# Optimization experiments

Hardware: AMD Instinct MI355X
Metric: run time of the kernel (lower is better)

## Reference

```python
import jax, jax.numpy as jnp
import numpy as np

HEADS = 4
DIM_HEAD = 32
EPS = 1e-5


def setup_inputs() -> dict:
    key = jax.random.key(0)
    ks = jax.random.split(key, 3)
    b, c, h, w = 32, 128, 128, 128
    hidden = HEADS * DIM_HEAD  # 128
    x = jax.random.normal(ks[0], (b, c, h, w), dtype=jnp.float32)
    Wqkv = jax.random.normal(ks[1], (3 * hidden, c), dtype=jnp.float32) * (1.0 / np.sqrt(c))
    Wout = jax.random.normal(ks[2], (c, hidden), dtype=jnp.float32) * (1.0 / np.sqrt(hidden))
    bout = jnp.zeros((c,), dtype=jnp.float32)
    g = jnp.ones((c,), dtype=jnp.float32)
    return {"x": x, "Wqkv": Wqkv, "Wout": Wout, "bout": bout, "g": g}


def reference(x, Wqkv, Wout, bout, g):
    b, c, h, w = x.shape
    n = h * w
    scale = DIM_HEAD ** -0.5
    # 1x1 conv (no bias) == channel GEMM
    qkv = jnp.einsum('oc,bchw->bohw', Wqkv, x)  # [b, 3*hidden, h, w]
    q, k, v = jnp.split(qkv, 3, axis=1)
    # b (h d) x y -> b h d n
    def to_heads(t):
        return t.reshape(b, HEADS, DIM_HEAD, n)
    q, k, v = to_heads(q), to_heads(k), to_heads(v)
    q = jax.nn.softmax(q, axis=-2) * scale   # softmax over per-head channel dim
    k = jax.nn.softmax(k, axis=-1)           # softmax over token dim
    v = v / n
    ctx = jnp.einsum('bhdn,bhen->bhde', k, v)   # [b, heads, d, e]
    out = jnp.einsum('bhde,bhdn->bhen', ctx, q)  # [b, heads, e, n]
    out = out.reshape(b, HEADS * DIM_HEAD, h, w)
    # output 1x1 conv with bias
    y = jnp.einsum('oc,bchw->bohw', Wout, out) + bout[None, :, None, None]
    # LayerNorm over channel dim (biased variance)
    mean = jnp.mean(y, axis=1, keepdims=True)
    var = jnp.var(y, axis=1, keepdims=True)
    return (y - mean) * jax.lax.rsqrt(var + EPS) * g[None, :, None, None]
```

## Files before the change

kernel.cpp:

```cpp
#include <hip/hip_runtime.h>
#include <math.h>


#define NCHUNK 64

typedef __attribute__((ext_vector_type(8))) short short8;
typedef __attribute__((ext_vector_type(4))) float f32x4;

__device__ __forceinline__ uint bf16r(float f) {
    uint u = __float_as_uint(f);
    return (u + 0x7FFFu + ((u >> 16) & 1u)) >> 16;
}
__device__ __forceinline__ float bf16f(uint h) { return __uint_as_float(h << 16); }
__device__ __forceinline__ uint2 bsplit(float f) {
    uint h = bf16r(f);
    float r = f - bf16f(h);
    return make_uint2(h, bf16r(r));
}
__device__ __forceinline__ uint2 bsplit_t(float f) {
    uint u = __float_as_uint(f);
    uint uh = u & 0xFFFF0000u;
    float r = f - __uint_as_float(uh);
    return make_uint2(uh >> 16, __float_as_uint(r) >> 16);
}
__device__ __forceinline__ uint bpack_t(float f) {
    uint u = __float_as_uint(f);
    uint uh = u & 0xFFFF0000u;
    float r = f - __uint_as_float(uh);
    return (uh >> 16) | (__float_as_uint(r) & 0xFFFF0000u);
}
__device__ __forceinline__ uint bpack(float f) {
    uint2 s = bsplit(f);
    return s.x | (s.y << 16);
}
__device__ __forceinline__ short8 lo8(uint4 a, uint4 b) {
    uint4 r;
    r.x = (a.x & 0xFFFFu) | (a.y << 16);
    r.y = (a.z & 0xFFFFu) | (a.w << 16);
    r.z = (b.x & 0xFFFFu) | (b.y << 16);
    r.w = (b.z & 0xFFFFu) | (b.w << 16);
    return __builtin_bit_cast(short8, r);
}
__device__ __forceinline__ short8 hi8(uint4 a, uint4 b) {
    uint4 r;
    r.x = (a.x >> 16) | (a.y & 0xFFFF0000u);
    r.y = (a.z >> 16) | (a.w & 0xFFFF0000u);
    r.z = (b.x >> 16) | (b.y & 0xFFFF0000u);
    r.w = (b.z >> 16) | (b.w & 0xFFFF0000u);
    return __builtin_bit_cast(short8, r);
}

__global__ __launch_bounds__(256)
void wsplit(const float* __restrict__ W, ushort* __restrict__ Wh,
            ushort* __restrict__ Wl, int n)
{
    const int base = (blockIdx.x * 256 + threadIdx.x) * 4;
    if (base + 3 < n) {
        const float4 f = *(const float4*)(W + base);
        const uint2 a = bsplit(f.x), b2 = bsplit(f.y), c = bsplit(f.z), d = bsplit(f.w);
        ushort4 hh; hh.x = (ushort)a.x; hh.y = (ushort)b2.x; hh.z = (ushort)c.x; hh.w = (ushort)d.x;
        ushort4 ll; ll.x = (ushort)a.y; ll.y = (ushort)b2.y; ll.z = (ushort)c.y; ll.w = (ushort)d.y;
        *(ushort4*)(Wh + base) = hh;
        *(ushort4*)(Wl + base) = ll;
    }
}

#define MFMA(A, B, C) __builtin_amdgcn_mfma_f32_16x16x32_bf16((A), (B), (C), 0, 0, 0)

__global__ __launch_bounds__(512, 1)
void la_k1(const float* __restrict__ x,
           const ushort* __restrict__ Wh, const ushort* __restrict__ Wl,
           float* __restrict__ Spart, float* __restrict__ Zpart)
{
    __shared__ __align__(16) char smb[163840];

    const int tid = threadIdx.x;
    const int b = blockIdx.y, chunk = blockIdx.x;
    const int w = tid >> 6, l = tid & 63;
    const int l15 = l & 15, lg = l >> 4;

    {
#pragma unroll
        for (int it = 0; it < 16; ++it) {
            const int q = tid + 512 * it;
            const int region = q >> 12;
            const int lin = (q & 4095) * 16;
            const int r = lin >> 8;
            const int dst = (region << 16) + (lin ^ ((r & 7) << 4));
            const ushort* src = (region ? Wl : Wh) + 128 * 128 + (lin >> 1);
            *(uint4*)(&smb[dst]) = *(const uint4*)src;
        }
    }

    f32x4 s2[2];
#pragma unroll
    for (int i = 0; i < 2; ++i) s2[i] = (f32x4){0.f, 0.f, 0.f, 0.f};
    float zrow[4];
#pragma unroll
    for (int i = 0; i < 4; ++i) zrow[i] = 0.f;

    const int hh = w >> 1, eh = w & 1;

    for (int t = 0; t < 8; ++t) {
        const int p0 = chunk * 256 + t * 32;
        {
            const float* xb = x + (size_t)b * 128 * 16384 + p0;
            const int cp = tid >> 3, j = tid & 7;
            const int pb = j * 4, c = cp * 2;
            const float4 a = *(const float4*)(xb + (size_t)c * 16384 + pb);
            const float4 bq = *(const float4*)(xb + (size_t)(c + 1) * 16384 + pb);
            const float av[4] = {a.x, a.y, a.z, a.w};
            const float bv[4] = {bq.x, bq.y, bq.z, bq.w};
#pragma unroll
            for (int pp = 0; pp < 4; ++pp) {
                const uint2 s0 = bsplit_t(av[pp]);
                const uint2 s1 = bsplit_t(bv[pp]);
                const int p = pb + pp;
                const int byt = (p * 256 + c * 2) ^ (((p ^ (p >> 3)) & 7) << 4);
                *(uint*)(&smb[131072 + byt])        = s0.x | (s1.x << 16);
                *(uint*)(&smb[131072 + 8192 + byt]) = s0.y | (s1.y << 16);
            }
        }
        __syncthreads();

        f32x4 acc[2][2];
#pragma unroll
        for (int rt = 0; rt < 2; ++rt)
#pragma unroll
            for (int ct = 0; ct < 2; ++ct) acc[rt][ct] = (f32x4){0.f, 0.f, 0.f, 0.f};
#pragma unroll
        for (int ks = 0; ks < 4; ++ks) {
            short8 Bh[2], Bl[2];
#pragma unroll
            for (int ct = 0; ct < 2; ++ct) {
                const int p = ct * 16 + l15;
                const int byt = (p * 256 + (ks * 32 + lg * 8) * 2) ^ (((p ^ (p >> 3)) & 7) << 4);
                Bh[ct] = *(const short8*)(&smb[131072 + byt]);
                Bl[ct] = *(const short8*)(&smb[131072 + 8192 + byt]);
            }
#pragma unroll
            for (int rt = 0; rt < 2; ++rt) {
                const int r = (w + rt * 8) * 16 + l15;
                const int abyt = (r * 256 + (ks * 32 + lg * 8) * 2) ^ ((r & 7) << 4);
                const short8 Ah_ = *(const short8*)(&smb[abyt]);
                const short8 Al_ = *(const short8*)(&smb[65536 + abyt]);
#pragma unroll
                for (int ct = 0; ct < 2; ++ct) {
                    acc[rt][ct] = MFMA(Ah_, Bh[ct], acc[rt][ct]);
                    acc[rt][ct] = MFMA(Ah_, Bl[ct], acc[rt][ct]);
                    acc[rt][ct] = MFMA(Al_, Bh[ct], acc[rt][ct]);
                }
            }
        }
        __syncthreads();

#pragma unroll
        for (int rt = 0; rt < 2; ++rt) {
            const bool isk = (rt == 0);
#pragma unroll
            for (int ct = 0; ct < 2; ++ct) {
                const int p = ct * 16 + l15;
#pragma unroll
                for (int i = 0; i < 4; ++i) {
                    float val = acc[rt][ct][i];
                    if (isk) {
                        val = expf(val);
                        zrow[i] += val;
                    }
                    const int r = w * 16 + lg * 4 + i;
                    const int byt = (r * 128 + p * 4) ^ ((r & 7) << 4);
                    *(uint*)(&smb[131072 + (isk ? 0 : 16384) + byt]) = bpack_t(val);
                }
            }
        }
        __syncthreads();

        {
            short8 A2h[2], A2l[2], B2h, B2l;
#pragma unroll
            for (int rt2 = 0; rt2 < 2; ++rt2) {
                const int r = hh * 32 + rt2 * 16 + l15;
                const int b0 = (r * 128 + lg * 32) ^ ((r & 7) << 4);
                const int b1 = (r * 128 + lg * 32 + 16) ^ ((r & 7) << 4);
                const uint4 q0 = *(const uint4*)(&smb[131072 + b0]);
                const uint4 q1 = *(const uint4*)(&smb[131072 + b1]);
                A2h[rt2] = lo8(q0, q1);
                A2l[rt2] = hi8(q0, q1);
            }
            {
                const int rv = hh * 32 + eh * 16 + l15;
                const int c0 = (rv * 128 + lg * 32) ^ ((rv & 7) << 4);
                const int c1 = (rv * 128 + lg * 32 + 16) ^ ((rv & 7) << 4);
                const uint4 r0 = *(const uint4*)(&smb[131072 + 16384 + c0]);
                const uint4 r1 = *(const uint4*)(&smb[131072 + 16384 + c1]);
                B2h = lo8(r0, r1);
                B2l = hi8(r0, r1);
            }
#pragma unroll
            for (int rt2 = 0; rt2 < 2; ++rt2) {
                s2[rt2] = MFMA(A2h[rt2], B2h, s2[rt2]);
                s2[rt2] = MFMA(A2h[rt2], B2l, s2[rt2]);
                s2[rt2] = MFMA(A2l[rt2], B2h, s2[rt2]);
            }
        }
        __syncthreads();
    }

    const size_t sbase = (((size_t)b * NCHUNK + chunk) * 4 + hh) * 1024;
#pragma unroll
    for (int rt2 = 0; rt2 < 2; ++rt2)
#pragma unroll
        for (int i = 0; i < 4; ++i) {
            const int d = rt2 * 16 + lg * 4 + i;
            const int e = eh * 16 + l15;
            Spart[sbase + d * 32 + e] = s2[rt2][i];
        }

#pragma unroll
    for (int i = 0; i < 4; ++i) {
        float z = zrow[i];
        z += __shfl_xor(z, 1, 64);
        z += __shfl_xor(z, 2, 64);
        z += __shfl_xor(z, 4, 64);
        z += __shfl_xor(z, 8, 64);
        if (l15 == 0)
            Zpart[((size_t)b * NCHUNK + chunk) * 128 + w * 16 + lg * 4 + i] = z;
    }
}

__global__ __launch_bounds__(256, 1)
void la_k1_reduce(const float* __restrict__ Spart, const float* __restrict__ Zpart,
                  uint* __restrict__ ctxT)
{
    const int tid = threadIdx.x;
    const int b  = blockIdx.x >> 2;
    const int hh = blockIdx.x & 3;
    const int d  = tid >> 3;
    const int e0 = (tid & 7) << 2;
    float sx = 0.f, sy = 0.f, sz = 0.f, sw = 0.f, z = 0.f;
    for (int ch = 0; ch < NCHUNK; ++ch) {
        const size_t base = (((size_t)b * NCHUNK + ch) * 4 + hh) * 32 + d;
        const float4 v = *(const float4*)(Spart + base * 32 + e0);
        sx += v.x; sy += v.y; sz += v.z; sw += v.w;
        z += Zpart[base];
    }
    const float inv = 1.0f / (z * 16384.0f);
    const size_t tb = (((size_t)b * 4 + hh) * 32) * 32 + d;
    ctxT[tb + (size_t)(e0 + 0) * 32] = bpack(sx * inv);
    ctxT[tb + (size_t)(e0 + 1) * 32] = bpack(sy * inv);
    ctxT[tb + (size_t)(e0 + 2) * 32] = bpack(sz * inv);
    ctxT[tb + (size_t)(e0 + 3) * 32] = bpack(sw * inv);
}

__device__ __forceinline__ int xswz64(int p, int cbyte) {
    return (p * 256 + cbyte) ^ (((p ^ (p >> 3)) & 7) << 4);
}

__global__ __launch_bounds__(256, 2)
void la_k2(const float* __restrict__ x,
           const ushort* __restrict__ Wqh, const ushort* __restrict__ Wql,
           const ushort* __restrict__ Woh, const ushort* __restrict__ Wol,
           const float* __restrict__ bout, const float* __restrict__ g,
           const uint* __restrict__ ctxT, float* __restrict__ outg)
{
    __shared__ __align__(16) char smb[66560];

    const int tid = threadIdx.x;
    const int b = blockIdx.y, chunk = blockIdx.x;
    const int p0 = chunk * 64;
    const int w = tid >> 6, l = tid & 63;
    const int l15 = l & 15, lg = l >> 4;
    const int ch2 = w >> 1;
    const int rp  = w & 1;

    short8 AqH[2][4], AqL[2][4];
#pragma unroll
    for (int t_ = 0; t_ < 2; ++t_)
#pragma unroll
        for (int ks = 0; ks < 4; ++ks) {
            const size_t aoff = (size_t)((2 * w + t_) * 16 + l15) * 128 + ks * 32 + lg * 8;
            AqH[t_][ks] = *(const short8*)(Wqh + aoff);
            AqL[t_][ks] = *(const short8*)(Wql + aoff);
        }

    {
        const float* xb = x + (size_t)b * 128 * 16384 + p0;
        const int j = tid & 15, gq = tid >> 4;
        const int pb = j * 4;
#pragma unroll
        for (int u = 0; u < 2; ++u) {
            const int cb = gq * 4 + u * 64;
            const float4 xv0 = *(const float4*)(xb + (size_t)(cb + 0) * 16384 + pb);
            const float4 xv1 = *(const float4*)(xb + (size_t)(cb + 1) * 16384 + pb);
            const float4 xv2 = *(const float4*)(xb + (size_t)(cb + 2) * 16384 + pb);
            const float4 xv3 = *(const float4*)(xb + (size_t)(cb + 3) * 16384 + pb);
            float rc[4][4];
            rc[0][0] = xv0.x; rc[0][1] = xv0.y; rc[0][2] = xv0.z; rc[0][3] = xv0.w;
            rc[1][0] = xv1.x; rc[1][1] = xv1.y; rc[1][2] = xv1.z; rc[1][3] = xv1.w;
            rc[2][0] = xv2.x; rc[2][1] = xv2.y; rc[2][2] = xv2.z; rc[2][3] = xv2.w;
            rc[3][0] = xv3.x; rc[3][1] = xv3.y; rc[3][2] = xv3.z; rc[3][3] = xv3.w;
#pragma unroll
            for (int pp = 0; pp < 4; ++pp) {
                const uint2 s0 = bsplit_t(rc[0][pp]);
                const uint2 s1 = bsplit_t(rc[1][pp]);
                const uint2 s2u = bsplit_t(rc[2][pp]);
                const uint2 s3 = bsplit_t(rc[3][pp]);
                const int p = pb + pp;
                const int byt = xswz64(p, cb * 2);
                *(uint2*)(&smb[byt])         = make_uint2(s0.x | (s1.x << 16), s2u.x | (s3.x << 16));
                *(uint2*)(&smb[16384 + byt]) = make_uint2(s0.y | (s1.y << 16), s2u.y | (s3.y << 16));
            }
        }
    }
    __syncthreads();

    f32x4 qacc[2][4];
#pragma unroll
    for (int t_ = 0; t_ < 2; ++t_)
#pragma unroll
        for (int ct = 0; ct < 4; ++ct) qacc[t_][ct] = (f32x4){0.f, 0.f, 0.f, 0.f};
#pragma unroll
    for (int ks = 0; ks < 4; ++ks) {
#pragma unroll
        for (int ct = 0; ct < 4; ++ct) {
            const int p = ct * 16 + l15;
            const int byt = xswz64(p, (ks * 32 + lg * 8) * 2);
            const short8 Bh_ = *(const short8*)(&smb[byt]);
            const short8 Bl_ = *(const short8*)(&smb[16384 + byt]);
#pragma unroll
            for (int t_ = 0; t_ < 2; ++t_) {
                qacc[t_][ct] = MFMA(AqH[t_][ks], Bh_, qacc[t_][ct]);
                qacc[t_][ct] = MFMA(AqH[t_][ks], Bl_, qacc[t_][ct]);
                qacc[t_][ct] = MFMA(AqL[t_][ks], Bh_, qacc[t_][ct]);
            }
        }
    }

    {
#pragma unroll
        for (int ct = 0; ct < 4; ++ct) {
            const int p = ct * 16 + l15;
            float vv[2][4];
            float m = -1e30f;
#pragma unroll
            for (int t_ = 0; t_ < 2; ++t_)
#pragma unroll
                for (int i = 0; i < 4; ++i) {
                    vv[t_][i] = qacc[t_][ct][i];
                    m = fmaxf(m, vv[t_][i]);
                }
            m = fmaxf(m, __shfl_xor(m, 16, 64));
            m = fmaxf(m, __shfl_xor(m, 32, 64));
            float s = 0.f;
#pragma unroll
            for (int t_ = 0; t_ < 2; ++t_)
#pragma unroll
                for (int i = 0; i < 4; ++i) {
                    vv[t_][i] = expf(vv[t_][i] - m);
                    s += vv[t_][i];
                }
            s += __shfl_xor(s, 16, 64);
            s += __shfl_xor(s, 32, 64);
            const float inv = 0.17677669529663687f / s;
            const int basep = (w * 64 + p) * 128;
            const int swzq = (p & 7) << 4;
#pragma unroll
            for (int t_ = 0; t_ < 2; ++t_) {
                uint4 pk;
                pk.x = bpack_t(vv[t_][0] * inv);
                pk.y = bpack_t(vv[t_][1] * inv);
                pk.z = bpack_t(vv[t_][2] * inv);
                pk.w = bpack_t(vv[t_][3] * inv);
                *(uint4*)(&smb[32768 + ((basep + (t_ * 16 + lg * 4) * 4) ^ swzq)]) = pk;
            }
        }
    }
    __syncthreads();

    {
#pragma unroll
        for (int jj = 0; jj < 4; ++jj) {
            const int rt = rp + 2 * jj;
            const int sh = rt >> 1;
            const int et = rt & 1;
            const size_t aidx = ((((size_t)b * 4 + sh) * 32) + et * 16 + l15) * 32 + lg * 8;
            const uint4 a0 = *(const uint4*)(ctxT + aidx);
            const uint4 a1 = *(const uint4*)(ctxT + aidx + 4);
            const short8 Ah_ = lo8(a0, a1);
            const short8 Al_ = hi8(a0, a1);
            f32x4 oacc[2];
#pragma unroll
            for (int ct = 0; ct < 2; ++ct) {
                oacc[ct] = (f32x4){0.f, 0.f, 0.f, 0.f};
                const int p = ch2 * 32 + ct * 16 + l15;
                const int bbq = (sh * 64 + p) * 128;
                const int swzq = (p & 7) << 4;
                const uint4 r0 = *(const uint4*)(&smb[32768 + ((bbq + lg * 32) ^ swzq)]);
                const uint4 r1 = *(const uint4*)(&smb[32768 + ((bbq + lg * 32 + 16) ^ swzq)]);
                const short8 Bh_ = lo8(r0, r1);
                const short8 Bl_ = hi8(r0, r1);
                oacc[ct] = MFMA(Ah_, Bh_, oacc[ct]);
                oacc[ct] = MFMA(Ah_, Bl_, oacc[ct]);
                oacc[ct] = MFMA(Al_, Bh_, oacc[ct]);
            }
#pragma unroll
            for (int ct = 0; ct < 2; ++ct) {
                const int p = ch2 * 32 + ct * 16 + l15;
                const int e0 = rt * 16 + lg * 4;
                uint4 pk;
                pk.x = bpack_t(oacc[ct][0]);
                pk.y = bpack_t(oacc[ct][1]);
                pk.z = bpack_t(oacc[ct][2]);
                pk.w = bpack_t(oacc[ct][3]);
                *(uint4*)(&smb[(p * 512 + e0 * 4) ^ ((p & 7) << 4)]) = pk;
            }
        }
    }
    __syncthreads();

    f32x4 yacc[4][2];
#pragma unroll
    for (int jj = 0; jj < 4; ++jj)
#pragma unroll
        for (int ct = 0; ct < 2; ++ct) yacc[jj][ct] = (f32x4){0.f, 0.f, 0.f, 0.f};
#pragma unroll
    for (int ks = 0; ks < 4; ++ks) {
        short8 Bh[2], Bl[2];
#pragma unroll
        for (int ct = 0; ct < 2; ++ct) {
            const int p = ch2 * 32 + ct * 16 + l15;
            const int bb = p * 512 + (ks * 32 + lg * 8) * 4;
            const int swz = (p & 7) << 4;
            const uint4 r0 = *(const uint4*)(&smb[(bb) ^ swz]);
            const uint4 r1 = *(const uint4*)(&smb[(bb + 16) ^ swz]);
            Bh[ct] = lo8(r0, r1);
            Bl[ct] = hi8(r0, r1);
        }
#pragma unroll
        for (int jj = 0; jj < 4; ++jj) {
            const int T = rp + 2 * jj;
            const size_t aoff = (size_t)(T * 16 + l15) * 128 + ks * 32 + lg * 8;
            const short8 Ah_ = *(const short8*)(Woh + aoff);
            const short8 Al_ = *(const short8*)(Wol + aoff);
#pragma unroll
            for (int ct = 0; ct < 2; ++ct) {
                yacc[jj][ct] = MFMA(Ah_, Bh[ct], yacc[jj][ct]);
                yacc[jj][ct] = MFMA(Ah_, Bl[ct], yacc[jj][ct]);
                yacc[jj][ct] = MFMA(Al_, Bh[ct], yacc[jj][ct]);
            }
        }
    }

    float4 bo[4], gv[4];
#pragma unroll
    for (int jj = 0; jj < 4; ++jj) {
        const int rbase = (rp + 2 * jj) * 16 + lg * 4;
        bo[jj] = *(const float4*)(bout + rbase);
        gv[jj] = *(const float4*)(g + rbase);
    }
#pragma unroll
    for (int jj = 0; jj < 4; ++jj)
#pragma unroll
        for (int ct = 0; ct < 2; ++ct) {
            yacc[jj][ct][0] += bo[jj].x;
            yacc[jj][ct][1] += bo[jj].y;
            yacc[jj][ct][2] += bo[jj].z;
            yacc[jj][ct][3] += bo[jj].w;
        }
    float* lnred = (float*)(smb + 65536);
    float sm[2], sq[2];
#pragma unroll
    for (int ct = 0; ct < 2; ++ct) {
        float s = 0.f, q = 0.f;
#pragma unroll
        for (int jj = 0; jj < 4; ++jj)
#pragma unroll
            for (int i = 0; i < 4; ++i) {
                const float yv = yacc[jj][ct][i];
                s += yv; q += yv * yv;
            }
        s += __shfl_xor(s, 16, 64); q += __shfl_xor(q, 16, 64);
        s += __shfl_xor(s, 32, 64); q += __shfl_xor(q, 32, 64);
        sm[ct] = s; sq[ct] = q;
    }
    if (lg == 0) {
#pragma unroll
        for (int ct = 0; ct < 2; ++ct) {
            const int p = ch2 * 32 + ct * 16 + l15;
            lnred[(p * 2 + rp) * 2 + 0] = sm[ct];
            lnred[(p * 2 + rp) * 2 + 1] = sq[ct];
        }
    }
    __syncthreads();
#pragma unroll
    for (int ct = 0; ct < 2; ++ct) {
        const int p = ch2 * 32 + ct * 16 + l15;
        const float st = lnred[(p * 2 + 0) * 2 + 0] + lnred[(p * 2 + 1) * 2 + 0];
        const float qt = lnred[(p * 2 + 0) * 2 + 1] + lnred[(p * 2 + 1) * 2 + 1];
        const float mean = st * (1.0f / 128.0f);
        const float var  = qt * (1.0f / 128.0f) - mean * mean;
        const float rstd = 1.0f / sqrtf(var + 1e-5f);
#pragma unroll
        for (int jj = 0; jj < 4; ++jj) {
            const int rbase = (rp + 2 * jj) * 16 + lg * 4;
            const float gg[4] = {gv[jj].x, gv[jj].y, gv[jj].z, gv[jj].w};
#pragma unroll
            for (int i = 0; i < 4; ++i) {
                const float val = (yacc[jj][ct][i] - mean) * rstd * gg[i];
                outg[((size_t)b * 128 + rbase + i) * 16384 + p0 + p] = val;
            }
        }
    }
}

extern "C" void kernel_launch(void* const* d_in, const int* in_sizes, int n_in,
                              void* d_out, int out_size, void* d_ws, size_t ws_size,
                              hipStream_t stream) {
    const float* x    = (const float*)d_in[0];
    const float* Wqkv = (const float*)d_in[1];
    const float* Wout = (const float*)d_in[2];
    const float* bout = (const float*)d_in[3];
    const float* g    = (const float*)d_in[4];
    float* out = (float*)d_out;

    float* Spart = (float*)d_ws;
    float* Zpart = Spart + (size_t)32 * NCHUNK * 4 * 32 * 32;
    uint*  ctxT  = (uint*)(Zpart + (size_t)32 * NCHUNK * 4 * 32);
    ushort* Wqh  = (ushort*)(ctxT + (size_t)32 * 4 * 32 * 32);
    ushort* Wql  = Wqh + 384 * 128;
    ushort* Woh  = Wql + 384 * 128;
    ushort* Wol  = Woh + 128 * 128;
    (void)in_sizes; (void)n_in; (void)out_size; (void)ws_size;

    wsplit<<<dim3(48), 256, 0, stream>>>(Wqkv, Wqh, Wql, 384 * 128);
    wsplit<<<dim3(16), 256, 0, stream>>>(Wout, Woh, Wol, 128 * 128);
    la_k1<<<dim3(NCHUNK, 32), 512, 0, stream>>>(x, Wqh, Wql, Spart, Zpart);
    la_k1_reduce<<<dim3(128), 256, 0, stream>>>(Spart, Zpart, ctxT);
    la_k2<<<dim3(256, 32), 256, 0, stream>>>(x, Wqh, Wql, Woh, Wol, bout, g, ctxT, out);
}
```

Measured before the change: 515.6 us.

## Fold context matrix into output projection weights per batch

Precomputes a per-batch matrix M = Wout·ctx in a new small kernel, so la_k2 applies a single GEMM on the softmaxed q instead of a ctx GEMM followed by the Wout GEMM. This removes one MFMA stage, a shared-memory round trip and a sync from the main kernel. The q tile is now stored as separate hi/lo bf16 planes in shared memory. In exchange it adds a serial per-batch kernel and per-batch weight reads, and reuses the Spart workspace to hold M.

```diff
diff --git a/kernel.cpp b/kernel.cpp
--- a/kernel.cpp
+++ b/kernel.cpp
@@ -28,10 +28,6 @@
     uint uh = u & 0xFFFF0000u;
     float r = f - __uint_as_float(uh);
     return (uh >> 16) | (__float_as_uint(r) & 0xFFFF0000u);
-}
-__device__ __forceinline__ uint bpack(float f) {
-    uint2 s = bsplit(f);
-    return s.x | (s.y << 16);
 }
 __device__ __forceinline__ short8 lo8(uint4 a, uint4 b) {
     uint4 r;
@@ -230,7 +226,7 @@
 
 __global__ __launch_bounds__(256, 1)
 void la_k1_reduce(const float* __restrict__ Spart, const float* __restrict__ Zpart,
-                  uint* __restrict__ ctxT)
+                  float* __restrict__ ctxF)
 {
     const int tid = threadIdx.x;
     const int b  = blockIdx.x >> 2;
@@ -245,11 +241,46 @@
         z += Zpart[base];
     }
     const float inv = 1.0f / (z * 16384.0f);
-    const size_t tb = (((size_t)b * 4 + hh) * 32) * 32 + d;
-    ctxT[tb + (size_t)(e0 + 0) * 32] = bpack(sx * inv);
-    ctxT[tb + (size_t)(e0 + 1) * 32] = bpack(sy * inv);
-    ctxT[tb + (size_t)(e0 + 2) * 32] = bpack(sz * inv);
-    ctxT[tb + (size_t)(e0 + 3) * 32] = bpack(sw * inv);
+    float4 r; r.x = sx * inv; r.y = sy * inv; r.z = sz * inv; r.w = sw * inv;
+    *(float4*)(ctxF + ((((size_t)b * 4 + hh) * 32 + d) << 5) + e0) = r;
+}
+
+__global__ __launch_bounds__(256, 1)
+void la_mk(const float* __restrict__ Wout, const float* __restrict__ ctxF,
+           ushort* __restrict__ Mh, ushort* __restrict__ Ml)
+{
+    __shared__ float ctxs[4096];
+    const int b = blockIdx.x;
+    const int tid = threadIdx.x;
+#pragma unroll
+    for (int i = 0; i < 4; ++i) {
+        const int idx = (tid + 256 * i) * 4;
+        *(float4*)(ctxs + idx) = *(const float4*)(ctxF + (size_t)b * 4096 + idx);
+    }
+    __syncthreads();
+    const int cp = tid & 127;
+    const int dh = tid >> 7;
+#pragma unroll
+    for (int hq = 0; hq < 2; ++hq) {
+        const int h = dh * 2 + hq;
+        float wrow[32];
+#pragma unroll
+        for (int e4 = 0; e4 < 8; ++e4) {
+            const float4 wv = *(const float4*)(Wout + cp * 128 + h * 32 + e4 * 4);
+            wrow[e4 * 4 + 0] = wv.x; wrow[e4 * 4 + 1] = wv.y;
+            wrow[e4 * 4 + 2] = wv.z; wrow[e4 * 4 + 3] = wv.w;
+        }
+        for (int d = 0; d < 32; ++d) {
+            float m = 0.f;
+#pragma unroll
+            for (int e = 0; e < 32; ++e)
+                m += wrow[e] * ctxs[h * 1024 + d * 32 + e];
+            const uint2 s = bsplit(m);
+            const size_t mo = (size_t)b * 16384 + cp * 128 + h * 32 + d;
+            Mh[mo] = (ushort)s.x;
+            Ml[mo] = (ushort)s.y;
+        }
+    }
 }
 
 __device__ __forceinline__ int xswz64(int p, int cbyte) {
@@ -259,9 +290,9 @@
 __global__ __launch_bounds__(256, 2)
 void la_k2(const float* __restrict__ x,
            const ushort* __restrict__ Wqh, const ushort* __restrict__ Wql,
-           const ushort* __restrict__ Woh, const ushort* __restrict__ Wol,
+           const ushort* __restrict__ Mh, const ushort* __restrict__ Ml,
            const float* __restrict__ bout, const float* __restrict__ g,
-           const uint* __restrict__ ctxT, float* __restrict__ outg)
+           float* __restrict__ outg)
 {
     __shared__ __align__(16) char smb[66560];
 
@@ -362,57 +393,16 @@
             s += __shfl_xor(s, 16, 64);
             s += __shfl_xor(s, 32, 64);
             const float inv = 0.17677669529663687f / s;
-            const int basep = (w * 64 + p) * 128;
-            const int swzq = (p & 7) << 4;
+            const int swzq = ((p >> 3) & 1) << 4;
 #pragma unroll
             for (int t_ = 0; t_ < 2; ++t_) {
-                uint4 pk;
-                pk.x = bpack_t(vv[t_][0] * inv);
-                pk.y = bpack_t(vv[t_][1] * inv);
-                pk.z = bpack_t(vv[t_][2] * inv);
-                pk.w = bpack_t(vv[t_][3] * inv);
-                *(uint4*)(&smb[32768 + ((basep + (t_ * 16 + lg * 4) * 4) ^ swzq)]) = pk;
-            }
-        }
-    }
-    __syncthreads();
-
-    {
-#pragma unroll
-        for (int jj = 0; jj < 4; ++jj) {
-            const int rt = rp + 2 * jj;
-            const int sh = rt >> 1;
-            const int et = rt & 1;
-            const size_t aidx = ((((size_t)b * 4 + sh) * 32) + et * 16 + l15) * 32 + lg * 8;
-            const uint4 a0 = *(const uint4*)(ctxT + aidx);
-            const uint4 a1 = *(const uint4*)(ctxT + aidx + 4);
-            const short8 Ah_ = lo8(a0, a1);
-            const short8 Al_ = hi8(a0, a1);
-            f32x4 oacc[2];
-#pragma unroll
-            for (int ct = 0; ct < 2; ++ct) {
-                oacc[ct] = (f32x4){0.f, 0.f, 0.f, 0.f};
-                const int p = ch2 * 32 + ct * 16 + l15;
-                const int bbq = (sh * 64 + p) * 128;
-                const int swzq = (p & 7) << 4;
-                const uint4 r0 = *(const uint4*)(&smb[32768 + ((bbq + lg * 32) ^ swzq)]);
-                const uint4 r1 = *(const uint4*)(&smb[32768 + ((bbq + lg * 32 + 16) ^ swzq)]);
-                const short8 Bh_ = lo8(r0, r1);
-                const short8 Bl_ = hi8(r0, r1);
-                oacc[ct] = MFMA(Ah_, Bh_, oacc[ct]);
-                oacc[ct] = MFMA(Ah_, Bl_, oacc[ct]);
-                oacc[ct] = MFMA(Al_, Bh_, oacc[ct]);
-            }
-#pragma unroll
-            for (int ct = 0; ct < 2; ++ct) {
-                const int p = ch2 * 32 + ct * 16 + l15;
-                const int e0 = rt * 16 + lg * 4;
-                uint4 pk;
-                pk.x = bpack_t(oacc[ct][0]);
-                pk.y = bpack_t(oacc[ct][1]);
-                pk.z = bpack_t(oacc[ct][2]);
-                pk.w = bpack_t(oacc[ct][3]);
-                *(uint4*)(&smb[(p * 512 + e0 * 4) ^ ((p & 7) << 4)]) = pk;
+                const uint2 a0 = bsplit_t(vv[t_][0] * inv);
+                const uint2 a1 = bsplit_t(vv[t_][1] * inv);
+                const uint2 a2 = bsplit_t(vv[t_][2] * inv);
+                const uint2 a3 = bsplit_t(vv[t_][3] * inv);
+                const int byt = (w * 4096 + p * 64 + (t_ * 16 + lg * 4) * 2) ^ swzq;
+                *(uint2*)(&smb[32768 + byt]) = make_uint2(a0.x | (a1.x << 16), a2.x | (a3.x << 16));
+                *(uint2*)(&smb[49152 + byt]) = make_uint2(a0.y | (a1.y << 16), a2.y | (a3.y << 16));
             }
         }
     }
@@ -429,19 +419,16 @@
 #pragma unroll
         for (int ct = 0; ct < 2; ++ct) {
             const int p = ch2 * 32 + ct * 16 + l15;
-            const int bb = p * 512 + (ks * 32 + lg * 8) * 4;
-            const int swz = (p & 7) << 4;
-            const uint4 r0 = *(const uint4*)(&smb[(bb) ^ swz]);
-            const uint4 r1 = *(const uint4*)(&smb[(bb + 16) ^ swz]);
-            Bh[ct] = lo8(r0, r1);
-            Bl[ct] = hi8(r0, r1);
+            const int byt = (ks * 4096 + p * 64 + lg * 16) ^ (((p >> 3) & 1) << 4);
+            Bh[ct] = *(const short8*)(&smb[32768 + byt]);
+            Bl[ct] = *(const short8*)(&smb[49152 + byt]);
         }
 #pragma unroll
         for (int jj = 0; jj < 4; ++jj) {
             const int T = rp + 2 * jj;
-            const size_t aoff = (size_t)(T * 16 + l15) * 128 + ks * 32 + lg * 8;
-            const short8 Ah_ = *(const short8*)(Woh + aoff);
-            const short8 Al_ = *(const short8*)(Wol + aoff);
+            const size_t aoff = (size_t)b * 16384 + (size_t)(T * 16 + l15) * 128 + ks * 32 + lg * 8;
+            const short8 Ah_ = *(const short8*)(Mh + aoff);
+            const short8 Al_ = *(const short8*)(Ml + aoff);
 #pragma unroll
             for (int ct = 0; ct < 2; ++ct) {
                 yacc[jj][ct] = MFMA(Ah_, Bh[ct], yacc[jj][ct]);
@@ -525,16 +512,16 @@
 
     float* Spart = (float*)d_ws;
     float* Zpart = Spart + (size_t)32 * NCHUNK * 4 * 32 * 32;
-    uint*  ctxT  = (uint*)(Zpart + (size_t)32 * NCHUNK * 4 * 32);
-    ushort* Wqh  = (ushort*)(ctxT + (size_t)32 * 4 * 32 * 32);
+    float* ctxF  = Zpart + (size_t)32 * NCHUNK * 4 * 32;
+    ushort* Wqh  = (ushort*)(ctxF + (size_t)32 * 4096);
     ushort* Wql  = Wqh + 384 * 128;
-    ushort* Woh  = Wql + 384 * 128;
-    ushort* Wol  = Woh + 128 * 128;
+    ushort* Mh   = (ushort*)Spart;
+    ushort* Ml   = Mh + (size_t)32 * 16384;
     (void)in_sizes; (void)n_in; (void)out_size; (void)ws_size;
 
     wsplit<<<dim3(48), 256, 0, stream>>>(Wqkv, Wqh, Wql, 384 * 128);
-    wsplit<<<dim3(16), 256, 0, stream>>>(Wout, Woh, Wol, 128 * 128);
     la_k1<<<dim3(NCHUNK, 32), 512, 0, stream>>>(x, Wqh, Wql, Spart, Zpart);
-    la_k1_reduce<<<dim3(128), 256, 0, stream>>>(Spart, Zpart, ctxT);
-    la_k2<<<dim3(256, 32), 256, 0, stream>>>(x, Wqh, Wql, Woh, Wol, bout, g, ctxT, out);
-}
+    la_k1_reduce<<<dim3(128), 256, 0, stream>>>(Spart, Zpart, ctxF);
+    la_mk<<<dim3(32), 256, 0, stream>>>(Wout, ctxF, Mh, Ml);
+    la_k2<<<dim3(256, 32), 256, 0, stream>>>(x, Wqh, Wql, Mh, Ml, bout, g, out);
+}
```

Measured after the change: 499.6 us. 3.1% less time.
